# Optimization experiments

Measured on AMD Instinct MI355X. Metric: run time of the kernel, lower is better.

The kernel has to match this reference:

```python
import jax, jax.numpy as jnp
import numpy as np

NUM_HEADS = 16
D_MODEL = 1024
D_KV = 64
NUM_BUCKETS = 32
MAX_DISTANCE = 128


def _relative_position_bucket(relative_position, num_buckets=NUM_BUCKETS, max_distance=MAX_DISTANCE):
    # faithful port of the torch static method (bidirectional variant)
    n = -relative_position
    nb = num_buckets // 2
    ret = (n < 0).astype(jnp.int32) * nb
    n = jnp.abs(n)
    max_exact = nb // 2
    is_small = n < max_exact
    # guard log(0); is_small branch covers n < max_exact anyway
    val_if_large = max_exact + (
        jnp.log(jnp.maximum(n, 1).astype(jnp.float32) / max_exact)
        / np.log(max_distance / max_exact)
        * (nb - max_exact)
    ).astype(jnp.int32)
    val_if_large = jnp.minimum(val_if_large, nb - 1)
    return ret + jnp.where(is_small, n, val_if_large)


def _compute_bias(seq_len, rel_bias):
    ctx = jnp.arange(seq_len)[:, None]
    mem = jnp.arange(seq_len)[None, :]
    bucket = _relative_position_bucket(mem - ctx)  # [S, S]
    values = rel_bias[bucket]                      # [S, S, H]
    return jnp.transpose(values, (2, 0, 1))[None]  # [1, H, S, S]


def setup_inputs() -> dict:
    key = jax.random.key(0)
    ks = jax.random.split(key, 6)
    B, S = 4, 1024
    scale = 1.0 / np.sqrt(D_MODEL)
    return {
        "hidden_states": jax.random.normal(ks[0], (B, S, D_MODEL), jnp.float32),
        "attention_mask": jnp.ones((B, 1, 1, S), jnp.int32),
        "Wq": jax.random.normal(ks[1], (NUM_HEADS * D_KV, D_MODEL), jnp.float32) * scale,
        "Wk": jax.random.normal(ks[2], (NUM_HEADS * D_KV, D_MODEL), jnp.float32) * scale,
        "Wv": jax.random.normal(ks[3], (NUM_HEADS * D_KV, D_MODEL), jnp.float32) * scale,
        "Wo": jax.random.normal(ks[4], (D_MODEL, NUM_HEADS * D_KV), jnp.float32) * scale,
        "rel_bias": jax.random.normal(ks[5], (NUM_BUCKETS, NUM_HEADS), jnp.float32),
    }


def reference(hidden_states, attention_mask, Wq, Wk, Wv, Wo, rel_bias):
    B, S, _ = hidden_states.shape
    # projections (Linear with bias=False: x @ W.T), reshape to [B, S, H, d_kv]
    q = jnp.einsum('bsd,ed->bse', hidden_states, Wq).reshape(B, S, NUM_HEADS, D_KV)
    k = jnp.einsum('bsd,ed->bse', hidden_states, Wk).reshape(B, S, NUM_HEADS, D_KV)
    v = jnp.einsum('bsd,ed->bse', hidden_states, Wv).reshape(B, S, NUM_HEADS, D_KV)
    scores = jnp.einsum('bqhd,bkhd->bhqk', q, k) / np.sqrt(D_KV)
    scores = scores + _compute_bias(S, rel_bias)
    scores = jnp.where(attention_mask == 0, jnp.float32(-1e9), scores)
    attn_weights = jax.nn.softmax(scores, axis=-1)  # dropout is identity at eval
    attn_output = jnp.einsum('bhqk,bkhd->bqhd', attn_weights, v).reshape(B, S, NUM_HEADS * D_KV)
    output = jnp.einsum('bse,de->bsd', attn_output, Wo)
    return output, attn_weights
```

## Files before the change

kernel.cpp:

```cpp
#include <hip/hip_runtime.h>
#include <hip/hip_bf16.h>

#define BB 4
#define SS 1024
#define HH 16
#define DK 64
#define DM 1024
#define MM (BB * SS)

typedef __attribute__((ext_vector_type(8))) short bh8_t;
typedef __attribute__((ext_vector_type(4))) float f4_t;

#define MFMA(a, b, c) __builtin_amdgcn_mfma_f32_16x16x32_bf16(a, b, c, 0, 0, 0)

__device__ __forceinline__ short f2bf(float f) {
    unsigned u = __builtin_bit_cast(unsigned, f);
    u = (u + 0x7FFFu + ((u >> 16) & 1u)) >> 16;
    return (short)u;
}
__device__ __forceinline__ float bf2f(short h) {
    unsigned u = ((unsigned)(unsigned short)h) << 16;
    return __builtin_bit_cast(float, u);
}

__device__ __forceinline__ void gl16(const short* g, short* l) {
    __builtin_amdgcn_global_load_lds(
        (const __attribute__((address_space(1))) void*)g,
        (__attribute__((address_space(3))) void*)l, 16, 0, 0);
}

__device__ __forceinline__ int rel_bucket(int rel) {
    int n = -rel;
    int ret = 0;
    if (n < 0) { ret = 16; n = -n; }
    int v;
    if (n < 8) {
        v = n;
    } else {
        float t = logf((float)n * 0.125f) / 2.7725887298583984f * 8.0f;
        v = 8 + (int)t;
        if (v > 15) v = 15;
    }
    return ret + v;
}

__global__ __launch_bounds__(256)
void k_split(const float* __restrict__ X, const float* __restrict__ Wq,
             const float* __restrict__ Wk, const float* __restrict__ Wv,
             const float* __restrict__ Wo, const float* __restrict__ rbv,
             short* __restrict__ Xh, short* __restrict__ Xl,
             short* __restrict__ Wqh, short* __restrict__ Wql,
             short* __restrict__ Wkh, short* __restrict__ Wkl,
             short* __restrict__ Wvh, short* __restrict__ Woh,
             float* __restrict__ biasT) {
    const long i = (long)blockIdx.x * 256 + threadIdx.x;
    if (i < 2097152) {
        const float* src;
        short* dh;
        short* dl = nullptr;
        long j = i;
        if (i < 1048576) { src = X; dh = Xh; dl = Xl; }
        else if (i < 1310720) { src = Wq; dh = Wqh; dl = Wql; j = i - 1048576; }
        else if (i < 1572864) { src = Wk; dh = Wkh; dl = Wkl; j = i - 1310720; }
        else if (i < 1835008) { src = Wv; dh = Wvh; j = i - 1572864; }
        else { src = Wo; dh = Woh; j = i - 1835008; }
        f4_t v = *(const f4_t*)(src + j * 4);
        short4 h, l;
        h.x = f2bf(v[0]); l.x = f2bf(v[0] - bf2f(h.x));
        h.y = f2bf(v[1]); l.y = f2bf(v[1] - bf2f(h.y));
        h.z = f2bf(v[2]); l.z = f2bf(v[2] - bf2f(h.z));
        h.w = f2bf(v[3]); l.w = f2bf(v[3] - bf2f(h.w));
        *(short4*)(dh + j * 4) = h;
        if (dl) *(short4*)(dl + j * 4) = l;
    } else if (i < 2105408) {
        const long j = i - 2097152;
        const int hd = (int)(j / 516);
        const int d0 = (int)(j % 516) * 4;
#pragma unroll
        for (int t = 0; t < 4; ++t) {
            const int dd = d0 + t;
            biasT[hd * 2064 + dd] = rbv[rel_bucket(dd - 1024) * HH + hd];
        }
    }
}

__global__ __launch_bounds__(256)
void k_proj(const short* __restrict__ Xh, const short* __restrict__ Xl,
            const short* __restrict__ Wqh, const short* __restrict__ Wql,
            const short* __restrict__ Wkh, const short* __restrict__ Wkl,
            const short* __restrict__ Wvh,
            short* __restrict__ Qh, short* __restrict__ Ql,
            short* __restrict__ Kh, short* __restrict__ Kl,
            short* __restrict__ Vt) {
    const int z = blockIdx.z;

    __shared__ short AhL[4096], AlL[4096], BhL[4096], BlL[4096];

    const int tid = threadIdx.x;
    const int m0 = blockIdx.y * 128, n0 = blockIdx.x * 128;
    const int wave = tid >> 6, lane = tid & 63;
    const int quad = lane >> 4, lm = lane & 15;
    const int wm = (wave >> 1) * 64, wn = (wave & 1) * 64;

    const int sr = wave * 32 + (lane >> 2);
    const int sc = (lane & 3) * 8;

    f4_t acc[4][4];
#pragma unroll
    for (int i = 0; i < 4; ++i)
#pragma unroll
        for (int j = 0; j < 4; ++j) acc[i][j] = (f4_t){0.f, 0.f, 0.f, 0.f};

    if (z < 2) {
        const short* Wh = z ? Wkh : Wqh;
        const short* Wl = z ? Wkl : Wql;
        short* Oh = z ? Kh : Qh;
        short* Ol = z ? Kl : Ql;

        for (int k0 = 0; k0 < DM; k0 += 32) {
            if (k0) __syncthreads();
#pragma unroll
            for (int j = 0; j < 2; ++j) {
                const int row = sr + j * 16;
                const int le = row * 32 + sc;
                gl16(Xh + (size_t)(m0 + row) * DM + k0 + sc, &AhL[le]);
                gl16(Xl + (size_t)(m0 + row) * DM + k0 + sc, &AlL[le]);
                gl16(Wh + (size_t)(n0 + row) * DM + k0 + sc, &BhL[le]);
                gl16(Wl + (size_t)(n0 + row) * DM + k0 + sc, &BlL[le]);
            }
            __syncthreads();

            bh8_t ah[4], al[4];
#pragma unroll
            for (int i = 0; i < 4; ++i) {
                ah[i] = *(const bh8_t*)&AhL[(wm + i * 16 + lm) * 32 + quad * 8];
                al[i] = *(const bh8_t*)&AlL[(wm + i * 16 + lm) * 32 + quad * 8];
            }
#pragma unroll
            for (int j = 0; j < 4; ++j) {
                bh8_t bhj = *(const bh8_t*)&BhL[(wn + j * 16 + lm) * 32 + quad * 8];
                bh8_t blj = *(const bh8_t*)&BlL[(wn + j * 16 + lm) * 32 + quad * 8];
#pragma unroll
                for (int i = 0; i < 4; ++i) {
                    acc[i][j] = MFMA(al[i], bhj, acc[i][j]);
                    acc[i][j] = MFMA(ah[i], blj, acc[i][j]);
                    acc[i][j] = MFMA(ah[i], bhj, acc[i][j]);
                }
            }
        }

#pragma unroll
        for (int i = 0; i < 4; ++i)
#pragma unroll
            for (int j = 0; j < 4; ++j)
#pragma unroll
                for (int g = 0; g < 4; ++g) {
                    const int row = m0 + wm + i * 16 + quad * 4 + g;
                    const int col = n0 + wn + j * 16 + lm;
                    const int b = row >> 10, s = row & 1023;
                    const int hd = col >> 6, dk = col & 63;
                    const float v = acc[i][j][g];
                    const short vh = f2bf(v);
                    const short vl = f2bf(v - bf2f(vh));
                    const size_t o = ((size_t)((b * HH + hd) * SS + s)) * DK + dk;
                    Oh[o] = vh;
                    Ol[o] = vl;
                }
    } else {
        for (int k0 = 0; k0 < DM; k0 += 32) {
            if (k0) __syncthreads();
#pragma unroll
            for (int j = 0; j < 2; ++j) {
                const int row = sr + j * 16;
                const int le = row * 32 + sc;
                gl16(Xh + (size_t)(m0 + row) * DM + k0 + sc, &AhL[le]);
                gl16(Wvh + (size_t)(n0 + row) * DM + k0 + sc, &BhL[le]);
            }
            __syncthreads();

            bh8_t ah[4];
#pragma unroll
            for (int i = 0; i < 4; ++i)
                ah[i] = *(const bh8_t*)&AhL[(wm + i * 16 + lm) * 32 + quad * 8];
#pragma unroll
            for (int j = 0; j < 4; ++j) {
                bh8_t bhj = *(const bh8_t*)&BhL[(wn + j * 16 + lm) * 32 + quad * 8];
#pragma unroll
                for (int i = 0; i < 4; ++i) acc[i][j] = MFMA(ah[i], bhj, acc[i][j]);
            }
        }

#pragma unroll
        for (int i = 0; i < 4; ++i)
#pragma unroll
            for (int j = 0; j < 4; ++j)
#pragma unroll
                for (int g = 0; g < 4; ++g) {
                    const int row = m0 + wm + i * 16 + quad * 4 + g;
                    const int col = n0 + wn + j * 16 + lm;
                    const int b = row >> 10, s = row & 1023;
                    const int hd = col >> 6, dk = col & 63;
                    Vt[((size_t)((b * HH + hd) * DK + dk)) * SS + s] = f2bf(acc[i][j][g]);
                }
    }
}

#define EPAD 1044

__global__ __launch_bounds__(512, 4)
void k_fused(const short* __restrict__ Qh, const short* __restrict__ Ql,
             const short* __restrict__ Kh, const short* __restrict__ Kl,
             const short* __restrict__ Vt, const int* __restrict__ mask,
             const float* __restrict__ biasT, float* __restrict__ P,
             short* __restrict__ AO) {
    __shared__ __align__(16) char smem[67328];
    float* E     = (float*)smem;
    float* redS  = (float*)smem;
    float* wsumS = (float*)(smem + 66816);

    const int tid = threadIdx.x;
    const int bid = blockIdx.x;
    const int swz = (bid & 7) * 512 + (bid >> 3);
    const int qb = swz & 63, bh = swz >> 6;
    const int b = bh >> 4, hd = bh & 15;
    const int q0 = qb * 16;
    const int wave = tid >> 6, lane = tid & 63;
    const int quad = lane >> 4, lm = lane & 15;

    const float* biasRow = biasT + hd * 2064 + 1024 - q0;
    const int* maskRow = mask + b * SS;

    bh8_t qah[2], qal[2];
#pragma unroll
    for (int ks = 0; ks < 2; ++ks) {
        const size_t qo = ((size_t)bh * SS + q0 + lm) * DK + ks * 32 + quad * 8;
        qah[ks] = *(const bh8_t*)(Qh + qo);
        qal[ks] = *(const bh8_t*)(Ql + qo);
    }

    float psum[4] = {0.f, 0.f, 0.f, 0.f};

    bh8_t kh[2][2][2], kl[2][2][2];
    {
        const int kb = wave * 128;
#pragma unroll
        for (int j = 0; j < 2; ++j)
#pragma unroll
            for (int ks = 0; ks < 2; ++ks) {
                const size_t ko =
                    ((size_t)bh * SS + kb + j * 16 + lm) * DK + ks * 32 + quad * 8;
                kh[0][j][ks] = *(const bh8_t*)(Kh + ko);
                kl[0][j][ks] = *(const bh8_t*)(Kl + ko);
            }
    }
#pragma unroll
    for (int kt = 0; kt < 4; ++kt) {
        const int cur = kt & 1;
        if (kt < 3) {
            const int kb2 = wave * 128 + (kt + 1) * 32;
#pragma unroll
            for (int j = 0; j < 2; ++j)
#pragma unroll
                for (int ks = 0; ks < 2; ++ks) {
                    const size_t ko =
                        ((size_t)bh * SS + kb2 + j * 16 + lm) * DK + ks * 32 + quad * 8;
                    kh[cur ^ 1][j][ks] = *(const bh8_t*)(Kh + ko);
                    kl[cur ^ 1][j][ks] = *(const bh8_t*)(Kl + ko);
                }
        }
        const int kb = wave * 128 + kt * 32;
        f4_t acc[2];
        acc[0] = (f4_t){0.f, 0.f, 0.f, 0.f};
        acc[1] = (f4_t){0.f, 0.f, 0.f, 0.f};
#pragma unroll
        for (int j = 0; j < 2; ++j)
#pragma unroll
            for (int ks = 0; ks < 2; ++ks) {
                acc[j] = MFMA(qal[ks], kh[cur][j][ks], acc[j]);
                acc[j] = MFMA(qah[ks], kl[cur][j][ks], acc[j]);
                acc[j] = MFMA(qah[ks], kh[cur][j][ks], acc[j]);
            }
#pragma unroll
        for (int j = 0; j < 2; ++j) {
            const int col = kb + j * 16 + lm;
            const int msk = maskRow[col];
#pragma unroll
            for (int g = 0; g < 4; ++g) {
                const int rl = quad * 4 + g;
                float s = acc[j][g] * 0.125f + biasRow[col - rl];
                s = (msk == 0) ? -1e9f : s;
                const float e = __expf(s);
                E[rl * EPAD + col] = e;
                psum[g] += e;
            }
        }
    }
#pragma unroll
    for (int g = 0; g < 4; ++g) {
        float p = psum[g];
        p += __shfl_xor(p, 1, 64);
        p += __shfl_xor(p, 2, 64);
        p += __shfl_xor(p, 4, 64);
        p += __shfl_xor(p, 8, 64);
        if (lm == 0) wsumS[(quad * 4 + g) * 8 + wave] = p;
    }

    bh8_t vb[2][4];
    {
        const int kg0 = wave * 128 + quad * 8;
#pragma unroll
        for (int f = 0; f < 4; ++f)
            vb[0][f] = *(const bh8_t*)(Vt + ((size_t)bh * DK + f * 16 + lm) * SS + kg0);
    }
    __syncthreads();

    auto invRow = [&](int r) -> float {
        f4_t a = *(const f4_t*)&wsumS[r * 8];
        f4_t c = *(const f4_t*)&wsumS[r * 8 + 4];
        return 1.0f / (a[0] + a[1] + a[2] + a[3] + c[0] + c[1] + c[2] + c[3]);
    };

    {
        const int c0 = (lane & 31) * 4;
        const int rh = lane >> 5;
#pragma unroll
        for (int u = 0; u < 8; ++u) {
            const int rr = u * 2 + rh;
            const float iv = invRow(rr);
            f4_t pv = *(const f4_t*)&E[rr * EPAD + wave * 128 + c0];
            pv[0] *= iv; pv[1] *= iv; pv[2] *= iv; pv[3] *= iv;
            __builtin_nontemporal_store(
                pv, (f4_t*)(P + ((size_t)bh * SS + q0 + rr) * SS + wave * 128 + c0));
        }
    }

    f4_t acc[4];
#pragma unroll
    for (int f = 0; f < 4; ++f) acc[f] = (f4_t){0.f, 0.f, 0.f, 0.f};

#pragma unroll
    for (int kk = 0; kk < 4; ++kk) {
        const int cur = kk & 1;
        const int kg = wave * 128 + kk * 32 + quad * 8;
        f4_t p0 = *(const f4_t*)&E[lm * EPAD + kg];
        f4_t p1 = *(const f4_t*)&E[lm * EPAD + kg + 4];
        if (kk < 3) {
            const int kg2 = wave * 128 + (kk + 1) * 32 + quad * 8;
#pragma unroll
            for (int f = 0; f < 4; ++f)
                vb[cur ^ 1][f] =
                    *(const bh8_t*)(Vt + ((size_t)bh * DK + f * 16 + lm) * SS + kg2);
        }
        bh8_t pa;
        pa[0] = f2bf(p0[0]); pa[1] = f2bf(p0[1]);
        pa[2] = f2bf(p0[2]); pa[3] = f2bf(p0[3]);
        pa[4] = f2bf(p1[0]); pa[5] = f2bf(p1[1]);
        pa[6] = f2bf(p1[2]); pa[7] = f2bf(p1[3]);
#pragma unroll
        for (int f = 0; f < 4; ++f) acc[f] = MFMA(pa, vb[cur][f], acc[f]);
    }

    float ivg[4];
#pragma unroll
    for (int g = 0; g < 4; ++g) ivg[g] = invRow(quad * 4 + g);

    asm volatile("s_waitcnt lgkmcnt(0)" ::: "memory");
    __builtin_amdgcn_sched_barrier(0);
    __builtin_amdgcn_s_barrier();
    __builtin_amdgcn_sched_barrier(0);

#pragma unroll
    for (int f = 0; f < 4; ++f)
#pragma unroll
        for (int g = 0; g < 4; ++g)
            redS[((size_t)wave * 16 + quad * 4 + g) * 64 + f * 16 + lm] =
                acc[f][g] * ivg[g];

    asm volatile("s_waitcnt lgkmcnt(0)" ::: "memory");
    __builtin_amdgcn_sched_barrier(0);
    __builtin_amdgcn_s_barrier();
    __builtin_amdgcn_sched_barrier(0);

    {
        const int flat = tid * 2;
        const int q = flat >> 6, dk = flat & 63;
        float s0 = 0.f, s1 = 0.f;
#pragma unroll
        for (int w = 0; w < 8; ++w) {
            s0 += redS[((size_t)w * 16 + q) * 64 + dk];
            s1 += redS[((size_t)w * 16 + q) * 64 + dk + 1];
        }
        short2 o;
        o.x = f2bf(s0);
        o.y = f2bf(s1);
        *(short2*)(AO + ((size_t)(b * SS + q0 + q)) * DM + hd * DK + dk) = o;
    }
}

__global__ __launch_bounds__(256)
void k_out(const short* __restrict__ A, const short* __restrict__ Woh,
           float* __restrict__ Out) {
    __shared__ short AsL[4096], BsL[4096];

    const int tid = threadIdx.x;
    const int m0 = blockIdx.y * 128, n0 = blockIdx.x * 128;
    const int wave = tid >> 6, lane = tid & 63;
    const int quad = lane >> 4, lm = lane & 15;
    const int wm = (wave >> 1) * 64, wn = (wave & 1) * 64;

    const int sr = wave * 32 + (lane >> 2);
    const int sc = (lane & 3) * 8;

    f4_t acc[4][4];
#pragma unroll
    for (int i = 0; i < 4; ++i)
#pragma unroll
        for (int j = 0; j < 4; ++j) acc[i][j] = (f4_t){0.f, 0.f, 0.f, 0.f};

    for (int k0 = 0; k0 < DM; k0 += 32) {
        if (k0) __syncthreads();
#pragma unroll
        for (int j = 0; j < 2; ++j) {
            const int row = sr + j * 16;
            const int le = row * 32 + sc;
            gl16(A + (size_t)(m0 + row) * DM + k0 + sc, &AsL[le]);
            gl16(Woh + (size_t)(n0 + row) * DM + k0 + sc, &BsL[le]);
        }
        __syncthreads();

        bh8_t ah[4];
#pragma unroll
        for (int i = 0; i < 4; ++i)
            ah[i] = *(const bh8_t*)&AsL[(wm + i * 16 + lm) * 32 + quad * 8];
#pragma unroll
        for (int j = 0; j < 4; ++j) {
            bh8_t bhj = *(const bh8_t*)&BsL[(wn + j * 16 + lm) * 32 + quad * 8];
#pragma unroll
            for (int i = 0; i < 4; ++i) acc[i][j] = MFMA(ah[i], bhj, acc[i][j]);
        }
    }

#pragma unroll
    for (int i = 0; i < 4; ++i)
#pragma unroll
        for (int j = 0; j < 4; ++j)
#pragma unroll
            for (int g = 0; g < 4; ++g)
                __builtin_nontemporal_store(
                    acc[i][j][g],
                    &Out[(size_t)(m0 + wm + i * 16 + quad * 4 + g) * DM + n0 + wn +
                         j * 16 + lm]);
}

extern "C" void kernel_launch(void* const* d_in, const int* in_sizes, int n_in,
                              void* d_out, int out_size, void* d_ws, size_t ws_size,
                              hipStream_t stream) {
    const float* X    = (const float*)d_in[0];
    const int*   mask = (const int*)d_in[1];
    const float* Wq   = (const float*)d_in[2];
    const float* Wk   = (const float*)d_in[3];
    const float* Wv   = (const float*)d_in[4];
    const float* Wo   = (const float*)d_in[5];
    const float* rb   = (const float*)d_in[6];

    float* out = (float*)d_out;
    float* P   = out + (size_t)BB * SS * DM;

    short* ws = (short*)d_ws;
    short* Qh  = ws;
    short* Ql  = ws + (size_t)4194304;
    short* Kh  = ws + (size_t)8388608;
    short* Kl  = ws + (size_t)12582912;
    short* Vt  = ws + (size_t)16777216;
    short* AO  = ws + (size_t)20971520;
    short* Xh  = ws + (size_t)25165824;
    short* Xl  = ws + (size_t)29360128;
    short* Wqh = ws + (size_t)33554432;
    short* Wql = ws + (size_t)34603008;
    short* Wkh = ws + (size_t)35651584;
    short* Wkl = ws + (size_t)36700160;
    short* Wvh = ws + (size_t)37748736;
    short* Woh = ws + (size_t)38797312;
    float* biasT = (float*)((char*)d_ws + 79691776);

    k_split<<<dim3(8225), 256, 0, stream>>>(X, Wq, Wk, Wv, Wo, rb, Xh, Xl, Wqh,
                                            Wql, Wkh, Wkl, Wvh, Woh, biasT);
    k_proj <<<dim3(8, 32, 3), 256, 0, stream>>>(Xh, Xl, Wqh, Wql, Wkh, Wkl, Wvh,
                                                Qh, Ql, Kh, Kl, Vt);
    k_fused<<<dim3(4096), 512, 0, stream>>>(Qh, Ql, Kh, Kl, Vt, mask, biasT, P, AO);
    k_out  <<<dim3(8, 32), 256, 0, stream>>>(AO, Woh, out);
}
```

Baseline: 554.5 us.

## Process 32 query rows per fused attention block with bf16 exp scratch

The fused attention kernel now handles 32 query rows per block instead of 16, halving the grid and reusing each loaded K and V fragment for two MFMA row tiles. The exponentiated scores are staged in shared memory as bf16 instead of fp32, so the larger tile fits in roughly the same LDS budget, and the P write-out is reorganised row-wise from that buffer. The explicit K/V register double-buffering is dropped in favour of simple loads plus s_setprio around MFMA blocks. The V-transpose store in the projection kernel is vectorised to short4. Storing exp values in bf16 before normalising P adds rounding error to the returned attention weights.

```diff
diff --git a/kernel.cpp b/kernel.cpp
--- a/kernel.cpp
+++ b/kernel.cpp
@@ -193,19 +193,22 @@
 #pragma unroll
         for (int i = 0; i < 4; ++i)
 #pragma unroll
-            for (int j = 0; j < 4; ++j)
-#pragma unroll
-                for (int g = 0; g < 4; ++g) {
-                    const int row = m0 + wm + i * 16 + quad * 4 + g;
-                    const int col = n0 + wn + j * 16 + lm;
-                    const int b = row >> 10, s = row & 1023;
-                    const int hd = col >> 6, dk = col & 63;
-                    Vt[((size_t)((b * HH + hd) * DK + dk)) * SS + s] = f2bf(acc[i][j][g]);
-                }
-    }
-}
-
-#define EPAD 1044
+            for (int j = 0; j < 4; ++j) {
+                const int row0 = m0 + wm + i * 16 + quad * 4;
+                const int col = n0 + wn + j * 16 + lm;
+                const int b = row0 >> 10, s0 = row0 & 1023;
+                const int hd = col >> 6, dk = col & 63;
+                short4 o;
+                o.x = f2bf(acc[i][j][0]);
+                o.y = f2bf(acc[i][j][1]);
+                o.z = f2bf(acc[i][j][2]);
+                o.w = f2bf(acc[i][j][3]);
+                *(short4*)&Vt[((size_t)((b * HH + hd) * DK + dk)) * SS + s0] = o;
+            }
+    }
+}
+
+#define EROW 1064
 
 __global__ __launch_bounds__(512, 4)
 void k_fused(const short* __restrict__ Qh, const short* __restrict__ Ql,
@@ -213,105 +216,94 @@
              const short* __restrict__ Vt, const int* __restrict__ mask,
              const float* __restrict__ biasT, float* __restrict__ P,
              short* __restrict__ AO) {
-    __shared__ __align__(16) char smem[67328];
-    float* E     = (float*)smem;
+    __shared__ __align__(16) char smem[69120];
+    short* E     = (short*)smem;
     float* redS  = (float*)smem;
-    float* wsumS = (float*)(smem + 66816);
+    float* wsumS = (float*)(smem + 68096);
 
     const int tid = threadIdx.x;
     const int bid = blockIdx.x;
-    const int swz = (bid & 7) * 512 + (bid >> 3);
-    const int qb = swz & 63, bh = swz >> 6;
+    const int swz = (bid & 7) * 256 + (bid >> 3);
+    const int qb = swz & 31, bh = swz >> 5;
     const int b = bh >> 4, hd = bh & 15;
-    const int q0 = qb * 16;
+    const int q0 = qb * 32;
     const int wave = tid >> 6, lane = tid & 63;
     const int quad = lane >> 4, lm = lane & 15;
 
     const float* biasRow = biasT + hd * 2064 + 1024 - q0;
     const int* maskRow = mask + b * SS;
 
-    bh8_t qah[2], qal[2];
-#pragma unroll
-    for (int ks = 0; ks < 2; ++ks) {
-        const size_t qo = ((size_t)bh * SS + q0 + lm) * DK + ks * 32 + quad * 8;
-        qah[ks] = *(const bh8_t*)(Qh + qo);
-        qal[ks] = *(const bh8_t*)(Ql + qo);
-    }
-
-    float psum[4] = {0.f, 0.f, 0.f, 0.f};
-
-    bh8_t kh[2][2][2], kl[2][2][2];
-    {
-        const int kb = wave * 128;
+    bh8_t qah[2][2], qal[2][2];
+#pragma unroll
+    for (int m = 0; m < 2; ++m)
+#pragma unroll
+        for (int ks = 0; ks < 2; ++ks) {
+            const size_t qo =
+                ((size_t)bh * SS + q0 + m * 16 + lm) * DK + ks * 32 + quad * 8;
+            qah[m][ks] = *(const bh8_t*)(Qh + qo);
+            qal[m][ks] = *(const bh8_t*)(Ql + qo);
+        }
+
+    float psum[2][4] = {{0.f, 0.f, 0.f, 0.f}, {0.f, 0.f, 0.f, 0.f}};
+
+#pragma unroll
+    for (int kt = 0; kt < 4; ++kt) {
+        const int kb = wave * 128 + kt * 32;
+        bh8_t kh[2][2], kl[2][2];
 #pragma unroll
         for (int j = 0; j < 2; ++j)
 #pragma unroll
             for (int ks = 0; ks < 2; ++ks) {
                 const size_t ko =
                     ((size_t)bh * SS + kb + j * 16 + lm) * DK + ks * 32 + quad * 8;
-                kh[0][j][ks] = *(const bh8_t*)(Kh + ko);
-                kl[0][j][ks] = *(const bh8_t*)(Kl + ko);
-            }
-    }
-#pragma unroll
-    for (int kt = 0; kt < 4; ++kt) {
-        const int cur = kt & 1;
-        if (kt < 3) {
-            const int kb2 = wave * 128 + (kt + 1) * 32;
-#pragma unroll
-            for (int j = 0; j < 2; ++j)
-#pragma unroll
-                for (int ks = 0; ks < 2; ++ks) {
-                    const size_t ko =
-                        ((size_t)bh * SS + kb2 + j * 16 + lm) * DK + ks * 32 + quad * 8;
-                    kh[cur ^ 1][j][ks] = *(const bh8_t*)(Kh + ko);
-                    kl[cur ^ 1][j][ks] = *(const bh8_t*)(Kl + ko);
+                kh[j][ks] = *(const bh8_t*)(Kh + ko);
+                kl[j][ks] = *(const bh8_t*)(Kl + ko);
+            }
+        f4_t acc[2][2];
+#pragma unroll
+        for (int m = 0; m < 2; ++m)
+#pragma unroll
+            for (int j = 0; j < 2; ++j) acc[m][j] = (f4_t){0.f, 0.f, 0.f, 0.f};
+        __builtin_amdgcn_s_setprio(1);
+#pragma unroll
+        for (int j = 0; j < 2; ++j)
+#pragma unroll
+            for (int ks = 0; ks < 2; ++ks)
+#pragma unroll
+                for (int m = 0; m < 2; ++m) {
+                    acc[m][j] = MFMA(qal[m][ks], kh[j][ks], acc[m][j]);
+                    acc[m][j] = MFMA(qah[m][ks], kl[j][ks], acc[m][j]);
+                    acc[m][j] = MFMA(qah[m][ks], kh[j][ks], acc[m][j]);
                 }
-        }
-        const int kb = wave * 128 + kt * 32;
-        f4_t acc[2];
-        acc[0] = (f4_t){0.f, 0.f, 0.f, 0.f};
-        acc[1] = (f4_t){0.f, 0.f, 0.f, 0.f};
-#pragma unroll
-        for (int j = 0; j < 2; ++j)
-#pragma unroll
-            for (int ks = 0; ks < 2; ++ks) {
-                acc[j] = MFMA(qal[ks], kh[cur][j][ks], acc[j]);
-                acc[j] = MFMA(qah[ks], kl[cur][j][ks], acc[j]);
-                acc[j] = MFMA(qah[ks], kh[cur][j][ks], acc[j]);
-            }
+        __builtin_amdgcn_s_setprio(0);
 #pragma unroll
         for (int j = 0; j < 2; ++j) {
             const int col = kb + j * 16 + lm;
             const int msk = maskRow[col];
 #pragma unroll
-            for (int g = 0; g < 4; ++g) {
-                const int rl = quad * 4 + g;
-                float s = acc[j][g] * 0.125f + biasRow[col - rl];
-                s = (msk == 0) ? -1e9f : s;
-                const float e = __expf(s);
-                E[rl * EPAD + col] = e;
-                psum[g] += e;
-            }
-        }
-    }
-#pragma unroll
-    for (int g = 0; g < 4; ++g) {
-        float p = psum[g];
-        p += __shfl_xor(p, 1, 64);
-        p += __shfl_xor(p, 2, 64);
-        p += __shfl_xor(p, 4, 64);
-        p += __shfl_xor(p, 8, 64);
-        if (lm == 0) wsumS[(quad * 4 + g) * 8 + wave] = p;
-    }
-
-    bh8_t vb[2][4];
-    {
-        const int kg0 = wave * 128 + quad * 8;
-#pragma unroll
-        for (int f = 0; f < 4; ++f)
-            vb[0][f] = *(const bh8_t*)(Vt + ((size_t)bh * DK + f * 16 + lm) * SS + kg0);
-    }
+            for (int m = 0; m < 2; ++m)
+#pragma unroll
+                for (int g = 0; g < 4; ++g) {
+                    const int rl = m * 16 + quad * 4 + g;
+                    float s = acc[m][j][g] * 0.125f + biasRow[col - rl];
+                    s = (msk == 0) ? -1e9f : s;
+                    const float e = __expf(s);
+                    E[rl * EROW + col] = f2bf(e);
+                    psum[m][g] += e;
+                }
+        }
+    }
+#pragma unroll
+    for (int m = 0; m < 2; ++m)
+#pragma unroll
+        for (int g = 0; g < 4; ++g) {
+            float p = psum[m][g];
+            p += __shfl_xor(p, 1, 64);
+            p += __shfl_xor(p, 2, 64);
+            p += __shfl_xor(p, 4, 64);
+            p += __shfl_xor(p, 8, 64);
+            if (lm == 0) wsumS[(m * 16 + quad * 4 + g) * 8 + wave] = p;
+        }
     __syncthreads();
 
     auto invRow = [&](int r) -> float {
@@ -321,48 +313,54 @@
     };
 
     {
-        const int c0 = (lane & 31) * 4;
-        const int rh = lane >> 5;
+        const int row = tid >> 4;
+        const int cb = (tid & 15) * 8;
+        const float iv = invRow(row);
+        float* Pr = P + ((size_t)bh * SS + q0 + row) * SS;
 #pragma unroll
         for (int u = 0; u < 8; ++u) {
-            const int rr = u * 2 + rh;
-            const float iv = invRow(rr);
-            f4_t pv = *(const f4_t*)&E[rr * EPAD + wave * 128 + c0];
-            pv[0] *= iv; pv[1] *= iv; pv[2] *= iv; pv[3] *= iv;
-            __builtin_nontemporal_store(
-                pv, (f4_t*)(P + ((size_t)bh * SS + q0 + rr) * SS + wave * 128 + c0));
-        }
-    }
-
-    f4_t acc[4];
-#pragma unroll
-    for (int f = 0; f < 4; ++f) acc[f] = (f4_t){0.f, 0.f, 0.f, 0.f};
+            const int c = cb + u * 128;
+            bh8_t ev = *(const bh8_t*)&E[row * EROW + c];
+            f4_t p0, p1;
+            p0[0] = bf2f(ev[0]) * iv; p0[1] = bf2f(ev[1]) * iv;
+            p0[2] = bf2f(ev[2]) * iv; p0[3] = bf2f(ev[3]) * iv;
+            p1[0] = bf2f(ev[4]) * iv; p1[1] = bf2f(ev[5]) * iv;
+            p1[2] = bf2f(ev[6]) * iv; p1[3] = bf2f(ev[7]) * iv;
+            __builtin_nontemporal_store(p0, (f4_t*)(Pr + c));
+            __builtin_nontemporal_store(p1, (f4_t*)(Pr + c + 4));
+        }
+    }
+
+    f4_t pacc[2][4];
+#pragma unroll
+    for (int m = 0; m < 2; ++m)
+#pragma unroll
+        for (int f = 0; f < 4; ++f) pacc[m][f] = (f4_t){0.f, 0.f, 0.f, 0.f};
 
 #pragma unroll
     for (int kk = 0; kk < 4; ++kk) {
-        const int cur = kk & 1;
         const int kg = wave * 128 + kk * 32 + quad * 8;
-        f4_t p0 = *(const f4_t*)&E[lm * EPAD + kg];
-        f4_t p1 = *(const f4_t*)&E[lm * EPAD + kg + 4];
-        if (kk < 3) {
-            const int kg2 = wave * 128 + (kk + 1) * 32 + quad * 8;
-#pragma unroll
-            for (int f = 0; f < 4; ++f)
-                vb[cur ^ 1][f] =
-                    *(const bh8_t*)(Vt + ((size_t)bh * DK + f * 16 + lm) * SS + kg2);
-        }
-        bh8_t pa;
-        pa[0] = f2bf(p0[0]); pa[1] = f2bf(p0[1]);
-        pa[2] = f2bf(p0[2]); pa[3] = f2bf(p0[3]);
-        pa[4] = f2bf(p1[0]); pa[5] = f2bf(p1[1]);
-        pa[6] = f2bf(p1[2]); pa[7] = f2bf(p1[3]);
-#pragma unroll
-        for (int f = 0; f < 4; ++f) acc[f] = MFMA(pa, vb[cur][f], acc[f]);
-    }
-
-    float ivg[4];
-#pragma unroll
-    for (int g = 0; g < 4; ++g) ivg[g] = invRow(quad * 4 + g);
+        bh8_t vbf[4];
+#pragma unroll
+        for (int f = 0; f < 4; ++f)
+            vbf[f] = *(const bh8_t*)(Vt + ((size_t)bh * DK + f * 16 + lm) * SS + kg);
+        bh8_t pa[2];
+#pragma unroll
+        for (int m = 0; m < 2; ++m)
+            pa[m] = *(const bh8_t*)&E[(m * 16 + lm) * EROW + kg];
+        __builtin_amdgcn_s_setprio(1);
+#pragma unroll
+        for (int f = 0; f < 4; ++f)
+#pragma unroll
+            for (int m = 0; m < 2; ++m) pacc[m][f] = MFMA(pa[m], vbf[f], pacc[m][f]);
+        __builtin_amdgcn_s_setprio(0);
+    }
+
+    float ivg[2][4];
+#pragma unroll
+    for (int m = 0; m < 2; ++m)
+#pragma unroll
+        for (int g = 0; g < 4; ++g) ivg[m][g] = invRow(m * 16 + quad * 4 + g);
 
     asm volatile("s_waitcnt lgkmcnt(0)" ::: "memory");
     __builtin_amdgcn_sched_barrier(0);
@@ -370,11 +368,13 @@
     __builtin_amdgcn_sched_barrier(0);
 
 #pragma unroll
-    for (int f = 0; f < 4; ++f)
-#pragma unroll
-        for (int g = 0; g < 4; ++g)
-            redS[((size_t)wave * 16 + quad * 4 + g) * 64 + f * 16 + lm] =
-                acc[f][g] * ivg[g];
+    for (int m = 0; m < 2; ++m)
+#pragma unroll
+        for (int f = 0; f < 4; ++f)
+#pragma unroll
+            for (int g = 0; g < 4; ++g)
+                redS[((size_t)wave * 32 + m * 16 + quad * 4 + g) * 64 + f * 16 + lm] =
+                    pacc[m][f][g] * ivg[m][g];
 
     asm volatile("s_waitcnt lgkmcnt(0)" ::: "memory");
     __builtin_amdgcn_sched_barrier(0);
@@ -382,18 +382,17 @@
     __builtin_amdgcn_sched_barrier(0);
 
     {
-        const int flat = tid * 2;
+        const int flat = tid * 4;
         const int q = flat >> 6, dk = flat & 63;
-        float s0 = 0.f, s1 = 0.f;
+        f4_t s = (f4_t){0.f, 0.f, 0.f, 0.f};
 #pragma unroll
         for (int w = 0; w < 8; ++w) {
-            s0 += redS[((size_t)w * 16 + q) * 64 + dk];
-            s1 += redS[((size_t)w * 16 + q) * 64 + dk + 1];
-        }
-        short2 o;
-        o.x = f2bf(s0);
-        o.y = f2bf(s1);
-        *(short2*)(AO + ((size_t)(b * SS + q0 + q)) * DM + hd * DK + dk) = o;
+            f4_t r = *(const f4_t*)&redS[((size_t)w * 32 + q) * 64 + dk];
+            s[0] += r[0]; s[1] += r[1]; s[2] += r[2]; s[3] += r[3];
+        }
+        short4 o;
+        o.x = f2bf(s[0]); o.y = f2bf(s[1]); o.z = f2bf(s[2]); o.w = f2bf(s[3]);
+        *(short4*)(AO + ((size_t)(b * SS + q0 + q)) * DM + hd * DK + dk) = o;
     }
 }
 
@@ -487,6 +486,6 @@
                                             Wql, Wkh, Wkl, Wvh, Woh, biasT);
     k_proj <<<dim3(8, 32, 3), 256, 0, stream>>>(Xh, Xl, Wqh, Wql, Wkh, Wkl, Wvh,
                                                 Qh, Ql, Kh, Kl, Vt);
-    k_fused<<<dim3(4096), 512, 0, stream>>>(Qh, Ql, Kh, Kl, Vt, mask, biasT, P, AO);
+    k_fused<<<dim3(2048), 512, 0, stream>>>(Qh, Ql, Kh, Kl, Vt, mask, biasT, P, AO);
     k_out  <<<dim3(8, 32), 256, 0, stream>>>(AO, Woh, out);
 }
```

Result: faster. 530.2 us (-4.4%).
